# Optimization experiments

Hardware: AMD Instinct MI355X
Metric: run time of the kernel (lower is better)

## Reference

```python
import jax, jax.numpy as jnp
import numpy as np

RH, RW = 40, 64          # render image height/width
SAM_HW = 64              # SAM ViT-H feature map spatial size
FEAT_DIM = 17            # voxel_feature_dim
GAUSSIAN_SEM_WEIGHT = 1.0


def nearest_resize(x, oh, ow):
    # torch F.interpolate mode='nearest': idx = floor(out_idx * in/out)
    ih, iw = x.shape[-2], x.shape[-1]
    ri = jnp.floor(jnp.arange(oh) * (ih / oh)).astype(jnp.int32)
    ci = jnp.floor(jnp.arange(ow) * (iw / ow)).astype(jnp.int32)
    return x[..., ri, :][..., ci]


def bilinear_resize(x, oh, ow):
    # torch bilinear, align_corners=False (half-pixel centers)
    ih, iw = x.shape[-2], x.shape[-1]
    def axis(isz, osz):
        src = (jnp.arange(osz, dtype=x.dtype) + 0.5) * (isz / osz) - 0.5
        i0 = jnp.clip(jnp.floor(src), 0, isz - 1).astype(jnp.int32)
        i1 = jnp.clip(i0 + 1, 0, isz - 1)
        w = jnp.clip(src - i0.astype(x.dtype), 0.0, 1.0)
        return i0, i1, w
    r0, r1, wr = axis(ih, oh)
    c0, c1, wc = axis(iw, ow)
    xr = x[..., r0, :] * (1 - wr)[:, None] + x[..., r1, :] * wr[:, None]
    return xr[..., c0] * (1 - wc) + xr[..., c1] * wc


def quat_to_rot(q):  # q: [N,4] normalized (w,x,y,z)
    w, x, y, z = q[:, 0], q[:, 1], q[:, 2], q[:, 3]
    R = jnp.stack([
        1 - 2 * (y * y + z * z), 2 * (x * y - w * z), 2 * (x * z + w * y),
        2 * (x * y + w * z), 1 - 2 * (x * x + z * z), 2 * (y * z - w * x),
        2 * (x * z - w * y), 2 * (y * z + w * x), 1 - 2 * (x * x + y * y)], -1)
    return R.reshape(-1, 3, 3)


def sam_proj(x, W1, b1, g1, be1, W2, b2, g2, be2, W3, b3):
    # Linear -> LayerNorm -> LeakyReLU (x2) -> Linear, all on last dim
    def ln(h, g, b):
        mu = h.mean(-1, keepdims=True)
        var = ((h - mu) ** 2).mean(-1, keepdims=True)
        return (h - mu) / jnp.sqrt(var + 1e-5) * g + b
    h = jax.nn.leaky_relu(ln(x @ W1.T + b1, g1, be1), 0.01)
    h = jax.nn.leaky_relu(ln(h @ W2.T + b2, g2, be2), 0.01)
    return h @ W3.T + b3


def render_feature_map(xyz, feats, opac, scal, quat, vm, intr):
    # Differentiable EWA Gaussian-splat feature rasterizer (3DGS-style math).
    N = xyz.shape[0]
    Rw, t = vm[:3, :3], vm[:3, 3]
    cam = xyz @ Rw.T + t                      # [N,3] camera coords
    x, y, z = cam[:, 0], cam[:, 1], cam[:, 2]
    fx, fy, cx, cy = intr[0], intr[1], intr[2], intr[3]
    zc = jnp.maximum(z, 1e-3)
    u = fx * x / zc + cx
    v = fy * y / zc + cy
    # 3D covariance Sigma = R S S^T R^T, transformed to camera then projected
    Rq = quat_to_rot(quat)
    M = Rq * scal[:, None, :]
    cov3 = M @ jnp.swapaxes(M, 1, 2)          # [N,3,3]
    covw = jnp.einsum('ij,njk,lk->nil', Rw, cov3, Rw)
    inv_z = 1.0 / zc
    zero = jnp.zeros_like(z)
    J = jnp.stack([
        jnp.stack([fx * inv_z, zero, -fx * x * inv_z ** 2], -1),
        jnp.stack([zero, fy * inv_z, -fy * y * inv_z ** 2], -1)], 1)  # [N,2,3]
    cov2 = jnp.einsum('nij,njk,nlk->nil', J, covw, J)
    a = cov2[:, 0, 0] + 0.3
    bq = cov2[:, 0, 1]
    cc = cov2[:, 1, 1] + 0.3
    det = a * cc - bq * bq
    A, Bc, Cc = cc / det, -bq / det, a / det   # conic (inverse 2D cov)
    xx, yy = jnp.meshgrid(jnp.arange(RW, dtype=xyz.dtype), jnp.arange(RH, dtype=xyz.dtype))
    px, py = xx.reshape(-1), yy.reshape(-1)    # [P]
    dx = u[:, None] - px[None, :]              # [N,P]
    dy = v[:, None] - py[None, :]
    power = -0.5 * (A[:, None] * dx * dx + Cc[:, None] * dy * dy) - Bc[:, None] * dx * dy
    alpha = jnp.minimum(0.99, opac * jnp.exp(jnp.minimum(power, 0.0)))
    alpha = alpha * (z > 0.2).astype(alpha.dtype)[:, None]
    # depth-sorted alpha compositing
    order = jnp.argsort(z)
    a_s = alpha[order]                         # [N,P]
    f_s = feats[order]                         # [N,C]
    T = jnp.concatenate([jnp.ones((1, a_s.shape[1]), a_s.dtype),
                         jnp.cumprod(1.0 - a_s, axis=0)[:-1]], axis=0)
    out = jnp.einsum('np,nc->cp', a_s * T, f_s)  # white_background=False -> bg 0
    return out.reshape(FEAT_DIM, RH, RW)


def _forward(voxel_feats, opacity, sam_embd, sam_features, sam_masks, viewmat,
             intrins, pc_xyz, scales, rots, W1, b1, g1, be1, W2, b2, g2, be2, W3, b3):
    B, C = viewmat.shape[0], viewmat.shape[1]
    scal = jnp.exp(scales)
    quat = rots / jnp.linalg.norm(rots, axis=-1, keepdims=True)
    proj = lambda x: sam_proj(x, W1, b1, g1, be1, W2, b2, g2, be2, W3, b3)
    loss_batch = 0.0
    for b in range(B):
        vf = voxel_feats[b].reshape(-1, FEAT_DIM)
        op = opacity[b].reshape(-1, 1)
        loss_c = 0.0
        for c in range(C):
            fmap = render_feature_map(pc_xyz, vf, op, scal, quat, viewmat[b, c], intrins[b, c])
            # use_sam: L1 between rendered map and projected SAM embedding
            se = nearest_resize(sam_embd[b, c], RH, RW)          # [256,RH,RW]
            sed = proj(se.transpose(1, 2, 0))                    # [RH,RW,17]
            loss_c = loss_c + jnp.abs(fmap.transpose(1, 2, 0) - sed).mean()
            # SAM mask contrastive loss
            sf = sam_features[b, c]                              # [256,64,64]
            ldf = proj(sf.reshape(256, -1).T).T.reshape(FEAT_DIM, SAM_HW, SAM_HW)
            masks = sam_masks[b, c]                              # [M,200,200]
            lsm = nearest_resize(masks, SAM_HW, SAM_HW)          # [M,64,64]
            proto = jnp.einsum('mhw,chw->mc', lsm, ldf)
            proto = proto / jnp.maximum(lsm.sum((1, 2)), 1e-6)[:, None]
            prob = jax.nn.sigmoid(jnp.einsum('mc,chw->mhw', proto, fmap))
            frm = bilinear_resize(masks, RH, RW)
            frm = jnp.where(frm <= 0.5, 0.0, frm)
            bce = frm * jnp.log(prob + 1e-8) + (1 - frm) * jnp.log(1 - prob + 1e-8)
            loss_c = loss_c - bce.mean()
        loss_batch = loss_batch + loss_c / C
    return loss_batch / B * GAUSSIAN_SEM_WEIGHT


def setup_inputs() -> dict:
    key = jax.random.key(0)
    ks = jax.random.split(key, 10)
    vs = 2.0
    gx1 = np.arange(-40.0, 40.0 + vs - 0.1, vs)
    gx = (gx1[:40] + gx1[1:41]) / 2
    gy = gx.copy()
    gz1 = np.arange(-2.4, 13.6 + vs - 0.1, vs)
    gz = (gz1[:8] + gz1[1:9]) / 2
    X, Y, Z = np.meshgrid(gx, gy, gz, indexing='ij')
    pc_xyz = np.stack([X, Y, Z], -1).reshape(-1, 3).astype(np.float32)
    N = pc_xyz.shape[0]  # 12800
    # regular grid: 3-NN mean squared dist = vs^2 -> scales = log(sqrt(vs^2))
    scales = np.full((N, 3), np.log(vs), np.float32)
    rots = np.zeros((N, 4), np.float32); rots[:, 0] = 1.0
    vm = np.zeros((1, 2, 4, 4), np.float32)
    vm[0, :, 0, 0] = vm[0, :, 1, 1] = vm[0, :, 2, 2] = vm[0, :, 3, 3] = 1.0
    vm[0, 0, :3, 3] = [0.0, 0.0, 60.0]
    vm[0, 1, :3, 3] = [2.0, -1.0, 62.0]
    intr = np.tile(np.array([32.0, 20.0, 32.0, 20.0], np.float32), (1, 2, 1))
    inp = {
        'voxel_feats': jax.random.normal(ks[0], (1, N, 17), jnp.float32) * 0.5,
        'opacity': jax.random.uniform(ks[1], (1, N, 1), jnp.float32) * 0.1,
        'sam_embd': jax.random.normal(ks[2], (1, 2, 256, 64, 64), jnp.float32),
        'sam_features': jax.random.normal(ks[3], (1, 2, 256, 64, 64), jnp.float32),
        'sam_masks': (jax.random.uniform(ks[4], (1, 2, 16, 200, 200)) < 0.3).astype(jnp.float32),
        'viewmat': jnp.asarray(vm), 'intrins': jnp.asarray(intr),
        'pc_xyz': jnp.asarray(pc_xyz), 'scales': jnp.asarray(scales), 'rots': jnp.asarray(rots),
        'W1': jax.random.normal(ks[5], (64, 256), jnp.float32) * 0.05,
        'b1': jnp.zeros((64,), jnp.float32),
        'g1': jnp.ones((64,), jnp.float32), 'be1': jnp.zeros((64,), jnp.float32),
        'W2': jax.random.normal(ks[6], (64, 64), jnp.float32) * 0.1,
        'b2': jnp.zeros((64,), jnp.float32),
        'g2': jnp.ones((64,), jnp.float32), 'be2': jnp.zeros((64,), jnp.float32),
        'W3': jax.random.normal(ks[7], (17, 64), jnp.float32) * 0.1,
        'b3': jnp.zeros((17,), jnp.float32),
    }
    return inp


def reference(voxel_feats, opacity, sam_embd, sam_features, sam_masks, viewmat,
              intrins, pc_xyz, scales, rots, W1, b1, g1, be1, W2, b2, g2, be2, W3, b3):
    return _forward(voxel_feats, opacity, sam_embd, sam_features, sam_masks, viewmat,
                    intrins, pc_xyz, scales, rots, W1, b1, g1, be1, W2, b2, g2, be2, W3, b3)
```

## Files before the change

### kernel.cpp

```cpp
#include <hip/hip_runtime.h>
#include <math.h>

#define NPTS   12800
#define P_PIX  2560
#define NC     64
#define CHUNK  200
#define RANK_CHUNK 800
#define MLP_PITCH 264

typedef short short8 __attribute__((ext_vector_type(8)));
typedef float f32x4 __attribute__((ext_vector_type(4)));

__device__ __forceinline__ unsigned short f2bf(float f) {
    unsigned int u = __float_as_uint(f);
    u += 0x7fffu + ((u >> 16) & 1u);
    return (unsigned short)(u >> 16);
}

__global__ __launch_bounds__(256) void init_kernel(int* rnk, float* out, int n) {
    int i = blockIdx.x * 256 + threadIdx.x;
    if (i < n) rnk[i] = 0;
    if (i == 0) out[0] = 0.0f;
}

__global__ __launch_bounds__(256) void prep_kernel(
    const float* __restrict__ xyz, const float* __restrict__ scales,
    const float* __restrict__ rots, const float* __restrict__ opacity,
    const float* __restrict__ viewmat, const float* __restrict__ intrins,
    unsigned long long* __restrict__ keys,
    float* __restrict__ pu, float* __restrict__ pv, float* __restrict__ prad,
    float* __restrict__ phA, float* __restrict__ phC, float* __restrict__ pnB,
    float* __restrict__ pop, int N) {
    int cam = blockIdx.y;
    int i = blockIdx.x * 256 + threadIdx.x;
    if (i >= N) return;
    const float* vm = viewmat + cam * 16;
    const float* it = intrins + cam * 4;
    float fx = it[0], fy = it[1], cx = it[2], cy = it[3];
    float R00 = vm[0], R01 = vm[1], R02 = vm[2], t0 = vm[3];
    float R10 = vm[4], R11 = vm[5], R12 = vm[6], t1 = vm[7];
    float R20 = vm[8], R21 = vm[9], R22 = vm[10], t2 = vm[11];
    float X = xyz[i * 3], Y = xyz[i * 3 + 1], Z = xyz[i * 3 + 2];
    float x = R00 * X + R01 * Y + R02 * Z + t0;
    float y = R10 * X + R11 * Y + R12 * Z + t1;
    float z = R20 * X + R21 * Y + R22 * Z + t2;
    float zc = fmaxf(z, 0.001f);
    float iz = 1.0f / zc;
    float u = fx * x * iz + cx;
    float v = fy * y * iz + cy;
    float qw = rots[i * 4], qx = rots[i * 4 + 1], qy = rots[i * 4 + 2], qz = rots[i * 4 + 3];
    float qn = 1.0f / sqrtf(qw * qw + qx * qx + qy * qy + qz * qz);
    qw *= qn; qx *= qn; qy *= qn; qz *= qn;
    float s0 = expf(scales[i * 3]), s1 = expf(scales[i * 3 + 1]), s2 = expf(scales[i * 3 + 2]);
    float Rq[3][3] = {
        {1 - 2 * (qy * qy + qz * qz), 2 * (qx * qy - qw * qz), 2 * (qx * qz + qw * qy)},
        {2 * (qx * qy + qw * qz), 1 - 2 * (qx * qx + qz * qz), 2 * (qy * qz - qw * qx)},
        {2 * (qx * qz - qw * qy), 2 * (qy * qz + qw * qx), 1 - 2 * (qx * qx + qy * qy)}};
    float M[3][3];
    #pragma unroll
    for (int r = 0; r < 3; ++r) { M[r][0] = Rq[r][0] * s0; M[r][1] = Rq[r][1] * s1; M[r][2] = Rq[r][2] * s2; }
    float c3[3][3];
    #pragma unroll
    for (int a = 0; a < 3; ++a)
        #pragma unroll
        for (int b = 0; b < 3; ++b)
            c3[a][b] = M[a][0] * M[b][0] + M[a][1] * M[b][1] + M[a][2] * M[b][2];
    float Rw[3][3] = {{R00, R01, R02}, {R10, R11, R12}, {R20, R21, R22}};
    float Wt[3][3];
    #pragma unroll
    for (int a = 0; a < 3; ++a)
        #pragma unroll
        for (int b = 0; b < 3; ++b)
            Wt[a][b] = Rw[a][0] * c3[0][b] + Rw[a][1] * c3[1][b] + Rw[a][2] * c3[2][b];
    float cw[3][3];
    #pragma unroll
    for (int a = 0; a < 3; ++a)
        #pragma unroll
        for (int b = 0; b < 3; ++b)
            cw[a][b] = Wt[a][0] * Rw[b][0] + Wt[a][1] * Rw[b][1] + Wt[a][2] * Rw[b][2];
    float j00 = fx * iz, j02 = -fx * x * iz * iz;
    float j11 = fy * iz, j12 = -fy * y * iz * iz;
    float c00 = j00 * j00 * cw[0][0] + 2.0f * j00 * j02 * cw[0][2] + j02 * j02 * cw[2][2];
    float c01 = j00 * j11 * cw[0][1] + j00 * j12 * cw[0][2] + j02 * j11 * cw[2][1] + j02 * j12 * cw[2][2];
    float c11 = j11 * j11 * cw[1][1] + 2.0f * j11 * j12 * cw[1][2] + j12 * j12 * cw[2][2];
    float a = c00 + 0.3f, bq = c01, cc = c11 + 0.3f;
    float det = a * cc - bq * bq;
    float A = cc / det, Bc = -bq / det, Cc = a / det;
    float lmin = 0.5f * ((A + Cc) - sqrtf((A - Cc) * (A - Cc) + 4.0f * Bc * Bc));
    lmin = fmaxf(lmin, 1e-20f);
    float opv = (z > 0.2f) ? opacity[i] : 0.0f;
    float rad = -1.0f;
    if (opv > 0.0f) {
        float tcut = logf(opv) + 18.42f;
        if (tcut > 0.0f) rad = sqrtf(2.0f * tcut / lmin);
    }
    int idx = cam * N + i;
    pu[idx] = u; pv[idx] = v; prad[idx] = rad;
    phA[idx] = -0.5f * A; phC[idx] = -0.5f * Cc; pnB[idx] = -Bc;
    pop[idx] = opv;
    unsigned int zb = __float_as_uint(z);
    zb = (zb & 0x80000000u) ? ~zb : (zb | 0x80000000u);
    keys[idx] = ((unsigned long long)zb << 32) | (unsigned int)i;
}

__global__ __launch_bounds__(256) void rank_kernel(const unsigned long long* __restrict__ keys,
                                                   int* __restrict__ rnk, int N) {
    __shared__ unsigned long long sk[RANK_CHUNK];
    int cam = blockIdx.z;
    const unsigned long long* K = keys + (size_t)cam * N;
    int jbase = blockIdx.y * RANK_CHUNK;
    int jcnt = min(RANK_CHUNK, N - jbase);
    for (int t = threadIdx.x; t < jcnt; t += 256) sk[t] = K[jbase + t];
    __syncthreads();
    int i = blockIdx.x * 256 + threadIdx.x;
    if (i >= N) return;
    unsigned long long ki = K[i];
    int cnt = 0;
    #pragma unroll 8
    for (int j = 0; j < jcnt; ++j) cnt += (sk[j] < ki) ? 1 : 0;
    if (cnt) atomicAdd(rnk + (size_t)cam * N + i, cnt);
}

__global__ __launch_bounds__(256) void scatter_kernel(
    const int* __restrict__ rnk,
    const float* __restrict__ pu, const float* __restrict__ pv, const float* __restrict__ prad,
    const float* __restrict__ phA, const float* __restrict__ phC, const float* __restrict__ pnB,
    const float* __restrict__ pop,
    const float* __restrict__ feats, float* __restrict__ rec, int N) {
    int cam = blockIdx.y;
    int i = blockIdx.x * 256 + threadIdx.x;
    if (i >= N) return;
    int idx = cam * N + i;
    int r = rnk[idx];
    float* d = rec + ((size_t)cam * N + r) * 24;
    d[0] = pu[idx]; d[1] = pv[idx]; d[2] = prad[idx]; d[3] = pop[idx];
    d[4] = phA[idx]; d[5] = phC[idx]; d[6] = pnB[idx];
    const float* f = feats + (size_t)i * 17;
    #pragma unroll
    for (int c = 0; c < 17; ++c) d[7 + c] = f[c];
}

__global__ __launch_bounds__(256) void build_kernel(const float* __restrict__ rec,
                                                    unsigned char* __restrict__ lists,
                                                    int* __restrict__ cnts, int N) {
    int gid = blockIdx.x * 4 + (threadIdx.x >> 6);
    int lane = threadIdx.x & 63;
    int cam = gid / (NC * 40);
    int rem = gid - cam * (NC * 40);
    int ch = rem / 40, row = rem - ch * 40;
    const float* rb = rec + ((size_t)cam * N + ch * CHUNK) * 24;
    unsigned char* L = lists + (size_t)gid * CHUNK;
    float py = (float)row;
    int cnt = 0;
    for (int g = 0; g < CHUNK; g += 64) {
        int n = g + lane;
        bool pass = false;
        if (n < CHUNK) {
            float v = rb[n * 24 + 1], rad = rb[n * 24 + 2];
            pass = fabsf(v - py) <= rad + 0.01f;
        }
        unsigned long long mask = __ballot(pass);
        int pre = __popcll(mask & ((1ull << lane) - 1ull));
        if (pass) L[cnt + pre] = (unsigned char)n;
        cnt += __popcll(mask);
    }
    if (lane == 0) cnts[gid] = cnt;
}

__global__ __launch_bounds__(256) void splat_kernel(const float* __restrict__ rec,
                                                    const unsigned char* __restrict__ lists,
                                                    const int* __restrict__ cnts,
                                                    float* __restrict__ part, int N) {
    __shared__ __align__(16) float4 sRec[CHUNK * 6];
    __shared__ unsigned char sList[4 * CHUNK];
    __shared__ int sCnt[4];
    int cam = blockIdx.z, ch = blockIdx.y, pg = blockIdx.x;
    int tid = threadIdx.x, lane = tid & 63, wv = tid >> 6;
    const float4* src = (const float4*)(rec + ((size_t)cam * N + ch * CHUNK) * 24);
    for (int t = tid; t < CHUNK * 6; t += 256) sRec[t] = src[t];
    int lid0 = (cam * NC + ch) * 40 + pg * 4;
    for (int t = tid; t < 4 * CHUNK; t += 256) {
        int w = t / CHUNK, i = t - w * CHUNK;
        sList[t] = lists[(size_t)(lid0 + w) * CHUNK + i];
    }
    if (tid < 4) sCnt[tid] = cnts[lid0 + tid];
    __syncthreads();
    int row = pg * 4 + wv;
    int cnt = sCnt[wv];
    float px = (float)lane, py = (float)row;
    float T = 1.0f;
    float acc[17];
    #pragma unroll
    for (int c = 0; c < 17; ++c) acc[c] = 0.0f;
    const unsigned char* myL = sList + wv * CHUNK;
    for (int i = 0; i < cnt; ++i) {
        int n = myL[i];
        const float4* rp = sRec + n * 6;
        float4 h  = rp[0];
        float4 b0 = rp[1];
        float dy = h.y - py;
        float dx = h.x - px;
        float hCdy2 = (b0.y * dy) * dy;
        float t1 = fmaf(b0.x, dx, b0.z * dy);
        float power = fminf(fmaf(t1, dx, hCdy2), 0.0f);
        float alpha = fminf(0.99f, h.w * __expf(power));
        float w = alpha * T;
        float4 q1 = rp[2], q2 = rp[3], q3 = rp[4], q4 = rp[5];
        acc[0]  = fmaf(w, b0.w, acc[0]);
        acc[1]  = fmaf(w, q1.x, acc[1]);  acc[2]  = fmaf(w, q1.y, acc[2]);
        acc[3]  = fmaf(w, q1.z, acc[3]);  acc[4]  = fmaf(w, q1.w, acc[4]);
        acc[5]  = fmaf(w, q2.x, acc[5]);  acc[6]  = fmaf(w, q2.y, acc[6]);
        acc[7]  = fmaf(w, q2.z, acc[7]);  acc[8]  = fmaf(w, q2.w, acc[8]);
        acc[9]  = fmaf(w, q3.x, acc[9]);  acc[10] = fmaf(w, q3.y, acc[10]);
        acc[11] = fmaf(w, q3.z, acc[11]); acc[12] = fmaf(w, q3.w, acc[12]);
        acc[13] = fmaf(w, q4.x, acc[13]); acc[14] = fmaf(w, q4.y, acc[14]);
        acc[15] = fmaf(w, q4.z, acc[15]); acc[16] = fmaf(w, q4.w, acc[16]);
        T *= (1.0f - alpha);
    }
    int p0 = row * 64 + lane;
    size_t base = ((size_t)(cam * NC + ch) * 18) * P_PIX;
    part[base + p0] = T;
    #pragma unroll
    for (int c = 0; c < 17; ++c)
        part[base + (size_t)(1 + c) * P_PIX + p0] = acc[c];
}

__global__ __launch_bounds__(256) void tpref_kernel(const float* __restrict__ part,
                                                    float* __restrict__ tpref) {
    int cam = blockIdx.y;
    int p = blockIdx.x * 256 + threadIdx.x;
    float T = 1.0f;
    #pragma unroll 8
    for (int k = 0; k < NC; ++k) {
        tpref[((size_t)(cam * NC + k)) * P_PIX + p] = T;
        T *= part[((size_t)(cam * NC + k) * 18) * P_PIX + p];
    }
}

__global__ __launch_bounds__(256) void combine_kernel(const float* __restrict__ part,
                                                      const float* __restrict__ tpref,
                                                      float* __restrict__ fmap) {
    int idx = blockIdx.x * 256 + threadIdx.x;
    if (idx >= 2 * 17 * P_PIX) return;
    int p = idx % P_PIX;
    int rem = idx / P_PIX;
    int c = rem % 17;
    int cam = rem / 17;
    float acc = 0.0f;
    #pragma unroll 8
    for (int k = 0; k < NC; ++k) {
        float Tp = tpref[((size_t)(cam * NC + k)) * P_PIX + p];
        float S = part[(((size_t)(cam * NC + k)) * 18 + 1 + c) * P_PIX + p];
        acc = fmaf(Tp, S, acc);
    }
    fmap[((size_t)cam * 17 + c) * P_PIX + p] = acc;
}

__global__ __launch_bounds__(256, 2) void mlp_kernel(
    const float* __restrict__ embd, const float* __restrict__ sfeat,
    const float* __restrict__ W1, const float* __restrict__ b1,
    const float* __restrict__ g1, const float* __restrict__ be1,
    const float* __restrict__ W2, const float* __restrict__ b2,
    const float* __restrict__ g2, const float* __restrict__ be2,
    const float* __restrict__ W3, const float* __restrict__ b3,
    float* __restrict__ sed, float* __restrict__ ldf) {
    __shared__ __align__(16) unsigned short smem[2 * 64 * MLP_PITCH];
    unsigned short* sX = smem;
    unsigned short* sW = smem + 64 * MLP_PITCH;
    int tid = threadIdx.x, lane = tid & 63, wv = tid >> 6;
    int m = lane & 15, kq = lane >> 4, q4 = kq * 4;
    int tile = blockIdx.x;
    const float* xbase;
    if (tile < 80) {
        int cam = tile / 40; int r = tile - cam * 40;
        int ri = (r * 8) / 5;
        xbase = embd + (size_t)cam * 256 * 4096 + ri * 64;
    } else {
        int tt = tile - 80; int cam = tt >> 6;
        xbase = sfeat + (size_t)cam * 256 * 4096 + (tt & 63) * 64;
    }
    const float4* xf4 = (const float4*)xbase;
    for (int idx = tid; idx < 4096; idx += 256) {
        int k = idx >> 4, q = idx & 15;
        float4 xv = xf4[(size_t)k * 1024 + q];
        int r = q * 4;
        sX[(r + 0) * MLP_PITCH + k] = f2bf(xv.x);
        sX[(r + 1) * MLP_PITCH + k] = f2bf(xv.y);
        sX[(r + 2) * MLP_PITCH + k] = f2bf(xv.z);
        sX[(r + 3) * MLP_PITCH + k] = f2bf(xv.w);
    }
    const float4* wf4 = (const float4*)W1;
    for (int idx = tid; idx < 4096; idx += 256) {
        float4 wvv = wf4[idx];
        int n = idx >> 6, kk = (idx & 63) * 4;
        uint2 pk;
        pk.x = (unsigned int)f2bf(wvv.x) | ((unsigned int)f2bf(wvv.y) << 16);
        pk.y = (unsigned int)f2bf(wvv.z) | ((unsigned int)f2bf(wvv.w) << 16);
        *(uint2*)&sW[n * MLP_PITCH + kk] = pk;
    }
    float b1v[4], g1v[4], be1v[4], b2v[4], g2v[4], be2v[4];
    #pragma unroll
    for (int nt = 0; nt < 4; ++nt) {
        int c = nt * 16 + m;
        b1v[nt] = b1[c]; g1v[nt] = g1[c]; be1v[nt] = be1[c];
        b2v[nt] = b2[c]; g2v[nt] = g2[c]; be2v[nt] = be2[c];
    }
    __syncthreads();
    f32x4 acc[4];
    #pragma unroll
    for (int nt = 0; nt < 4; ++nt) acc[nt] = (f32x4){0.f, 0.f, 0.f, 0.f};
    const unsigned short* aptr = sX + (wv * 16 + m) * MLP_PITCH + kq * 8;
    const unsigned short* bptr = sW + m * MLP_PITCH + kq * 8;
    #pragma unroll
    for (int ks = 0; ks < 8; ++ks) {
        short8 af = *(const short8*)(aptr + ks * 32);
        #pragma unroll
        for (int nt = 0; nt < 4; ++nt) {
            short8 bf = *(const short8*)(bptr + nt * 16 * MLP_PITCH + ks * 32);
            acc[nt] = __builtin_amdgcn_mfma_f32_16x16x32_bf16(af, bf, acc[nt], 0, 0, 0);
        }
    }
    __syncthreads();
    unsigned short* hbuf  = smem + wv * 16 * 72;
    unsigned short* hbuf2 = smem + (4 + wv) * 16 * 72;
    unsigned short* W2b = sW;
    unsigned short* W3b = sW + 64 * 72;
    for (int i = tid; i < 4096; i += 256)
        W2b[(i >> 6) * 72 + (i & 63)] = f2bf(W2[i]);
    for (int i = tid; i < 2048; i += 256) {
        int n = i >> 6, k = i & 63;
        W3b[n * 72 + k] = (n < 17) ? f2bf(W3[n * 64 + k]) : 0;
    }
    #pragma unroll
    for (int rg = 0; rg < 4; ++rg) {
        float h0 = acc[0][rg] + b1v[0], h1 = acc[1][rg] + b1v[1];
        float h2 = acc[2][rg] + b1v[2], h3 = acc[3][rg] + b1v[3];
        float s = (h0 + h1) + (h2 + h3);
        s += __shfl_xor(s, 1); s += __shfl_xor(s, 2);
        s += __shfl_xor(s, 4); s += __shfl_xor(s, 8);
        float mu = s * (1.0f / 64.0f);
        float d0 = h0 - mu, d1 = h1 - mu, d2 = h2 - mu, d3 = h3 - mu;
        float vs = (d0 * d0 + d1 * d1) + (d2 * d2 + d3 * d3);
        vs += __shfl_xor(vs, 1); vs += __shfl_xor(vs, 2);
        vs += __shfl_xor(vs, 4); vs += __shfl_xor(vs, 8);
        float rstd = 1.0f / sqrtf(vs * (1.0f / 64.0f) + 1e-5f);
        float hn0 = d0 * rstd * g1v[0] + be1v[0]; hn0 = fmaxf(hn0, 0.01f * hn0);
        float hn1 = d1 * rstd * g1v[1] + be1v[1]; hn1 = fmaxf(hn1, 0.01f * hn1);
        float hn2 = d2 * rstd * g1v[2] + be1v[2]; hn2 = fmaxf(hn2, 0.01f * hn2);
        float hn3 = d3 * rstd * g1v[3] + be1v[3]; hn3 = fmaxf(hn3, 0.01f * hn3);
        int rr = (q4 + rg) * 72 + m;
        hbuf[rr] = f2bf(hn0); hbuf[rr + 16] = f2bf(hn1);
        hbuf[rr + 32] = f2bf(hn2); hbuf[rr + 48] = f2bf(hn3);
    }
    __syncthreads();
    f32x4 acc2[4];
    #pragma unroll
    for (int nt = 0; nt < 4; ++nt) acc2[nt] = (f32x4){0.f, 0.f, 0.f, 0.f};
    const unsigned short* a2p = hbuf + m * 72 + kq * 8;
    #pragma unroll
    for (int ks = 0; ks < 2; ++ks) {
        short8 af = *(const short8*)(a2p + ks * 32);
        #pragma unroll
        for (int nt = 0; nt < 4; ++nt) {
            short8 bf = *(const short8*)(W2b + (nt * 16 + m) * 72 + kq * 8 + ks * 32);
            acc2[nt] = __builtin_amdgcn_mfma_f32_16x16x32_bf16(af, bf, acc2[nt], 0, 0, 0);
        }
    }
    #pragma unroll
    for (int rg = 0; rg < 4; ++rg) {
        float h0 = acc2[0][rg] + b2v[0], h1 = acc2[1][rg] + b2v[1];
        float h2 = acc2[2][rg] + b2v[2], h3 = acc2[3][rg] + b2v[3];
        float s = (h0 + h1) + (h2 + h3);
        s += __shfl_xor(s, 1); s += __shfl_xor(s, 2);
        s += __shfl_xor(s, 4); s += __shfl_xor(s, 8);
        float mu = s * (1.0f / 64.0f);
        float d0 = h0 - mu, d1 = h1 - mu, d2 = h2 - mu, d3 = h3 - mu;
        float vs = (d0 * d0 + d1 * d1) + (d2 * d2 + d3 * d3);
        vs += __shfl_xor(vs, 1); vs += __shfl_xor(vs, 2);
        vs += __shfl_xor(vs, 4); vs += __shfl_xor(vs, 8);
        float rstd = 1.0f / sqrtf(vs * (1.0f / 64.0f) + 1e-5f);
        float hn0 = d0 * rstd * g2v[0] + be2v[0]; hn0 = fmaxf(hn0, 0.01f * hn0);
        float hn1 = d1 * rstd * g2v[1] + be2v[1]; hn1 = fmaxf(hn1, 0.01f * hn1);
        float hn2 = d2 * rstd * g2v[2] + be2v[2]; hn2 = fmaxf(hn2, 0.01f * hn2);
        float hn3 = d3 * rstd * g2v[3] + be2v[3]; hn3 = fmaxf(hn3, 0.01f * hn3);
        int rr = (q4 + rg) * 72 + m;
        hbuf2[rr] = f2bf(hn0); hbuf2[rr + 16] = f2bf(hn1);
        hbuf2[rr + 32] = f2bf(hn2); hbuf2[rr + 48] = f2bf(hn3);
    }
    f32x4 acc3[2];
    acc3[0] = (f32x4){0.f, 0.f, 0.f, 0.f};
    acc3[1] = (f32x4){0.f, 0.f, 0.f, 0.f};
    const unsigned short* a3p = hbuf2 + m * 72 + kq * 8;
    #pragma unroll
    for (int ks = 0; ks < 2; ++ks) {
        short8 af = *(const short8*)(a3p + ks * 32);
        #pragma unroll
        for (int nt = 0; nt < 2; ++nt) {
            short8 bf = *(const short8*)(W3b + (nt * 16 + m) * 72 + kq * 8 + ks * 32);
            acc3[nt] = __builtin_amdgcn_mfma_f32_16x16x32_bf16(af, bf, acc3[nt], 0, 0, 0);
        }
    }
    #pragma unroll
    for (int nt = 0; nt < 2; ++nt) {
        int c = nt * 16 + m;
        if (c < 17) {
            float b3v = b3[c];
            #pragma unroll
            for (int rg = 0; rg < 4; ++rg) {
                int row = tile * 64 + wv * 16 + q4 + rg;
                float val = acc3[nt][rg] + b3v;
                if (row < 5120) {
                    int cam = row / 2560; int p = row - cam * 2560;
                    sed[((size_t)cam * 2560 + p) * 17 + c] = val;
                } else {
                    int rr = row - 5120; int cam = rr >> 12; int t = rr & 4095;
                    ldf[((size_t)cam * 17 + c) * 4096 + t] = val;
                }
            }
        }
    }
}

__global__ __launch_bounds__(256) void proto_kernel(const float* __restrict__ masks,
                                                    const float* __restrict__ ldf,
                                                    float* __restrict__ proto) {
    int cam = blockIdx.y, m = blockIdx.x;
    const float* M = masks + ((size_t)cam * 16 + m) * 40000;
    float acc[18];
    #pragma unroll
    for (int j = 0; j < 18; ++j) acc[j] = 0.0f;
    for (int t = threadIdx.x; t < 4096; t += 256) {
        int h = t >> 6, w = t & 63;
        int rh = (h * 25) >> 3, rw = (w * 25) >> 3;
        float lv = M[rh * 200 + rw];
        if (lv != 0.0f) {
            acc[17] += lv;
            const float* L = ldf + (size_t)cam * 17 * 4096 + t;
            #pragma unroll
            for (int c = 0; c < 17; ++c) acc[c] = fmaf(lv, L[(size_t)c * 4096], acc[c]);
        }
    }
    __shared__ float red[4][18];
    int lane = threadIdx.x & 63, wv = threadIdx.x >> 6;
    #pragma unroll
    for (int j = 0; j < 18; ++j) {
        float v = acc[j];
        #pragma unroll
        for (int o = 32; o; o >>= 1) v += __shfl_xor(v, o);
        if (lane == 0) red[wv][j] = v;
    }
    __syncthreads();
    if (threadIdx.x < 17) {
        float sacc = red[0][threadIdx.x] + red[1][threadIdx.x] + red[2][threadIdx.x] + red[3][threadIdx.x];
        float ms = red[0][17] + red[1][17] + red[2][17] + red[3][17];
        proto[((size_t)cam * 16 + m) * 17 + threadIdx.x] = sacc / fmaxf(ms, 1e-6f);
    }
}

__device__ __forceinline__ void block_atomic_add(float v, float* target) {
    #pragma unroll
    for (int o = 32; o; o >>= 1) v += __shfl_xor(v, o);
    __shared__ float sred[4];
    int lane = threadIdx.x & 63, wv = threadIdx.x >> 6;
    if (lane == 0) sred[wv] = v;
    __syncthreads();
    if (threadIdx.x == 0) atomicAdd(target, sred[0] + sred[1] + sred[2] + sred[3]);
}

__global__ __launch_bounds__(256) void bce_kernel(const float* __restrict__ masks,
                                                  const float* __restrict__ proto,
                                                  const float* __restrict__ fmap,
                                                  float* __restrict__ out) {
    int idx = blockIdx.x * 256 + threadIdx.x;
    int p = idx % P_PIX;
    int rem = idx / P_PIX;
    int m = rem & 15, cam = rem >> 4;
    const float* pr = proto + ((size_t)cam * 16 + m) * 17;
    float sdot = 0;
    #pragma unroll
    for (int c = 0; c < 17; ++c)
        sdot = fmaf(pr[c], fmap[((size_t)cam * 17 + c) * P_PIX + p], sdot);
    float prob = 1.0f / (1.0f + expf(-sdot));
    int px = p & 63, py = p >> 6;
    float src_r = (py + 0.5f) * 5.0f - 0.5f;
    float src_c = (px + 0.5f) * 3.125f - 0.5f;
    int r0 = (int)fminf(fmaxf(floorf(src_r), 0.0f), 199.0f);
    int r1 = min(r0 + 1, 199);
    float wr = fminf(fmaxf(src_r - (float)r0, 0.0f), 1.0f);
    int c0 = (int)fminf(fmaxf(floorf(src_c), 0.0f), 199.0f);
    int c1 = min(c0 + 1, 199);
    float wc = fminf(fmaxf(src_c - (float)c0, 0.0f), 1.0f);
    const float* M = masks + ((size_t)cam * 16 + m) * 40000;
    float v00 = M[r0 * 200 + c0], v01 = M[r0 * 200 + c1];
    float v10 = M[r1 * 200 + c0], v11 = M[r1 * 200 + c1];
    float xr0 = v00 * (1.0f - wr) + v10 * wr;
    float xr1 = v01 * (1.0f - wr) + v11 * wr;
    float frm = xr0 * (1.0f - wc) + xr1 * wc;
    frm = (frm <= 0.5f) ? 0.0f : frm;
    float bce = frm * logf(prob + 1e-8f) + (1.0f - frm) * logf(1.0f - prob + 1e-8f);
    block_atomic_add(bce * (-1.0f / (16.0f * 2560.0f * 2.0f)), out);
}

__global__ __launch_bounds__(256) void l1_kernel(const float* __restrict__ fmap,
                                                 const float* __restrict__ sed,
                                                 float* __restrict__ out) {
    int idx = blockIdx.x * 256 + threadIdx.x;
    float ssum = 0;
    if (idx < 2 * P_PIX) {
        int p = idx % P_PIX, cam = idx / P_PIX;
        #pragma unroll
        for (int c = 0; c < 17; ++c) {
            float dv = fmap[((size_t)cam * 17 + c) * P_PIX + p] - sed[((size_t)cam * P_PIX + p) * 17 + c];
            ssum += fabsf(dv);
        }
    }
    block_atomic_add(ssum * (1.0f / (43520.0f * 2.0f)), out);
}

extern "C" void kernel_launch(void* const* d_in, const int* in_sizes, int n_in,
                              void* d_out, int out_size, void* d_ws, size_t ws_size,
                              hipStream_t stream) {
    const float* voxel_feats = (const float*)d_in[0];
    const float* opacity     = (const float*)d_in[1];
    const float* sam_embd    = (const float*)d_in[2];
    const float* sam_features= (const float*)d_in[3];
    const float* sam_masks   = (const float*)d_in[4];
    const float* viewmat     = (const float*)d_in[5];
    const float* intrins     = (const float*)d_in[6];
    const float* pc_xyz      = (const float*)d_in[7];
    const float* scales      = (const float*)d_in[8];
    const float* rots        = (const float*)d_in[9];
    const float* W1 = (const float*)d_in[10], *b1 = (const float*)d_in[11];
    const float* g1 = (const float*)d_in[12], *be1 = (const float*)d_in[13];
    const float* W2 = (const float*)d_in[14], *b2 = (const float*)d_in[15];
    const float* g2 = (const float*)d_in[16], *be2 = (const float*)d_in[17];
    const float* W3 = (const float*)d_in[18], *b3 = (const float*)d_in[19];
    float* out = (float*)d_out;
    const int N = in_sizes[7] / 3;

    char* w = (char*)d_ws;
    size_t off = 0;
    auto alloc = [&](size_t bytes) -> void* {
        off = (off + 255) & ~(size_t)255;
        void* p = w + off; off += bytes; return p;
    };
    int* rnk  = (int*)alloc((size_t)2 * N * sizeof(int));
    unsigned long long* keys = (unsigned long long*)alloc((size_t)2 * N * 8);
    float* params = (float*)alloc((size_t)7 * 2 * N * 4);
    float* pu  = params,           *pv  = params + 2 * N,  *prad = params + 4 * N;
    float* phA = params + 6 * N,   *phC = params + 8 * N,  *pnB  = params + 10 * N;
    float* pop = params + 12 * N;
    float* rec   = (float*)alloc((size_t)2 * N * 24 * 4);
    float* part  = (float*)alloc((size_t)2 * NC * 18 * P_PIX * 4);
    float* tpref = (float*)alloc((size_t)2 * NC * P_PIX * 4);
    float* fmap  = (float*)alloc((size_t)2 * 17 * P_PIX * 4);
    float* sed   = (float*)alloc((size_t)2 * P_PIX * 17 * 4);
    float* ldf   = (float*)alloc((size_t)2 * 17 * 4096 * 4);
    float* proto = (float*)alloc((size_t)2 * 16 * 17 * 4);
    unsigned char* lists = (unsigned char*)alloc((size_t)2 * NC * 40 * CHUNK);
    int* cnts = (int*)alloc((size_t)2 * NC * 40 * sizeof(int));

    init_kernel<<<(2 * N + 255) / 256, 256, 0, stream>>>(rnk, out, 2 * N);
    dim3 gprep((N + 255) / 256, 2);
    prep_kernel<<<gprep, 256, 0, stream>>>(pc_xyz, scales, rots, opacity, viewmat, intrins,
                                           keys, pu, pv, prad, phA, phC, pnB, pop, N);
    dim3 grank((N + 255) / 256, (N + RANK_CHUNK - 1) / RANK_CHUNK, 2);
    rank_kernel<<<grank, 256, 0, stream>>>(keys, rnk, N);
    scatter_kernel<<<gprep, 256, 0, stream>>>(rnk, pu, pv, prad, phA, phC, pnB, pop,
                                              voxel_feats, rec, N);
    build_kernel<<<2 * NC * 40 / 4, 256, 0, stream>>>(rec, lists, cnts, N);
    dim3 gsplat(10, NC, 2);
    splat_kernel<<<gsplat, 256, 0, stream>>>(rec, lists, cnts, part, N);
    dim3 gtp(P_PIX / 256, 2);
    tpref_kernel<<<gtp, 256, 0, stream>>>(part, tpref);
    combine_kernel<<<(2 * 17 * P_PIX + 255) / 256, 256, 0, stream>>>(part, tpref, fmap);
    mlp_kernel<<<208, 256, 0, stream>>>(sam_embd, sam_features, W1, b1, g1, be1,
                                        W2, b2, g2, be2, W3, b3, sed, ldf);
    dim3 gproto(16, 2);
    proto_kernel<<<gproto, 256, 0, stream>>>(sam_masks, ldf, proto);
    bce_kernel<<<(2 * 16 * P_PIX) / 256, 256, 0, stream>>>(sam_masks, proto, fmap, out);
    l1_kernel<<<(2 * P_PIX + 255) / 256, 256, 0, stream>>>(fmap, sed, out);
}
```

Before: 236.3 us.

## Fuse init/tpref/l1 kernels, enlarge chunks, register-tile rank, compact splat record

Folds the rank-buffer zeroing into prep, the transmittance prefix into combine, and the L1 loss into the BCE kernel, removing three launches and the tpref buffer. Halves the depth-chunk count by doubling chunk size, which moves list indices to 16-bit, and adds a separate compact (v, radius) array so the list-build pass reads 8 bytes per point instead of strided records. The rank kernel now compares each shared key against four per-thread keys to raise reuse, and the splat inner loop uses packed two-wide FMAs over a tighter record layout. BCE switches to fast exp/log intrinsics, which slightly changes numerics, and larger chunks mean longer serial per-wave loops with fewer blocks.

```diff
diff --git a/kernel.cpp b/kernel.cpp
--- a/kernel.cpp
+++ b/kernel.cpp
@@ -3,24 +3,20 @@
 
 #define NPTS   12800
 #define P_PIX  2560
-#define NC     64
-#define CHUNK  200
+#define NC     32
+#define CHUNK  400
 #define RANK_CHUNK 800
+#define RT     4
 #define MLP_PITCH 264
 
 typedef short short8 __attribute__((ext_vector_type(8)));
 typedef float f32x4 __attribute__((ext_vector_type(4)));
+typedef float f32x2 __attribute__((ext_vector_type(2)));
 
 __device__ __forceinline__ unsigned short f2bf(float f) {
     unsigned int u = __float_as_uint(f);
     u += 0x7fffu + ((u >> 16) & 1u);
     return (unsigned short)(u >> 16);
-}
-
-__global__ __launch_bounds__(256) void init_kernel(int* rnk, float* out, int n) {
-    int i = blockIdx.x * 256 + threadIdx.x;
-    if (i < n) rnk[i] = 0;
-    if (i == 0) out[0] = 0.0f;
 }
 
 __global__ __launch_bounds__(256) void prep_kernel(
@@ -30,10 +26,13 @@
     unsigned long long* __restrict__ keys,
     float* __restrict__ pu, float* __restrict__ pv, float* __restrict__ prad,
     float* __restrict__ phA, float* __restrict__ phC, float* __restrict__ pnB,
-    float* __restrict__ pop, int N) {
+    float* __restrict__ pop, int* __restrict__ rnk, float* __restrict__ out, int N) {
     int cam = blockIdx.y;
     int i = blockIdx.x * 256 + threadIdx.x;
     if (i >= N) return;
+    int idx = cam * N + i;
+    rnk[idx] = 0;
+    if (idx == 0) out[0] = 0.0f;
     const float* vm = viewmat + cam * 16;
     const float* it = intrins + cam * 4;
     float fx = it[0], fy = it[1], cx = it[2], cy = it[3];
@@ -94,7 +93,6 @@
         float tcut = logf(opv) + 18.42f;
         if (tcut > 0.0f) rad = sqrtf(2.0f * tcut / lmin);
     }
-    int idx = cam * N + i;
     pu[idx] = u; pv[idx] = v; prad[idx] = rad;
     phA[idx] = -0.5f * A; phC[idx] = -0.5f * Cc; pnB[idx] = -Bc;
     pop[idx] = opv;
@@ -112,13 +110,26 @@
     int jcnt = min(RANK_CHUNK, N - jbase);
     for (int t = threadIdx.x; t < jcnt; t += 256) sk[t] = K[jbase + t];
     __syncthreads();
-    int i = blockIdx.x * 256 + threadIdx.x;
-    if (i >= N) return;
-    unsigned long long ki = K[i];
-    int cnt = 0;
-    #pragma unroll 8
-    for (int j = 0; j < jcnt; ++j) cnt += (sk[j] < ki) ? 1 : 0;
-    if (cnt) atomicAdd(rnk + (size_t)cam * N + i, cnt);
+    int i0 = blockIdx.x * (256 * RT) + threadIdx.x;
+    unsigned long long ki[RT];
+    int cnt[RT];
+    #pragma unroll
+    for (int t = 0; t < RT; ++t) {
+        int i = i0 + t * 256;
+        ki[t] = (i < N) ? K[i] : 0xFFFFFFFFFFFFFFFFull;
+        cnt[t] = 0;
+    }
+    #pragma unroll 4
+    for (int j = 0; j < jcnt; ++j) {
+        unsigned long long kj = sk[j];
+        #pragma unroll
+        for (int t = 0; t < RT; ++t) cnt[t] += (kj < ki[t]) ? 1 : 0;
+    }
+    #pragma unroll
+    for (int t = 0; t < RT; ++t) {
+        int i = i0 + t * 256;
+        if (i < N && cnt[t]) atomicAdd(rnk + (size_t)cam * N + i, cnt[t]);
+    }
 }
 
 __global__ __launch_bounds__(256) void scatter_kernel(
@@ -126,119 +137,110 @@
     const float* __restrict__ pu, const float* __restrict__ pv, const float* __restrict__ prad,
     const float* __restrict__ phA, const float* __restrict__ phC, const float* __restrict__ pnB,
     const float* __restrict__ pop,
-    const float* __restrict__ feats, float* __restrict__ rec, int N) {
+    const float* __restrict__ feats, float* __restrict__ rec, float2* __restrict__ vr, int N) {
     int cam = blockIdx.y;
     int i = blockIdx.x * 256 + threadIdx.x;
     if (i >= N) return;
     int idx = cam * N + i;
     int r = rnk[idx];
     float* d = rec + ((size_t)cam * N + r) * 24;
-    d[0] = pu[idx]; d[1] = pv[idx]; d[2] = prad[idx]; d[3] = pop[idx];
-    d[4] = phA[idx]; d[5] = phC[idx]; d[6] = pnB[idx];
+    d[0] = pu[idx]; d[1] = pv[idx]; d[2] = pop[idx]; d[3] = phA[idx];
+    d[4] = phC[idx]; d[5] = pnB[idx];
     const float* f = feats + (size_t)i * 17;
     #pragma unroll
-    for (int c = 0; c < 17; ++c) d[7 + c] = f[c];
-}
-
-__global__ __launch_bounds__(256) void build_kernel(const float* __restrict__ rec,
-                                                    unsigned char* __restrict__ lists,
+    for (int c = 0; c < 17; ++c) d[6 + c] = f[c];
+    d[23] = 0.0f;
+    vr[(size_t)cam * N + r] = make_float2(pv[idx], prad[idx]);
+}
+
+__global__ __launch_bounds__(256) void build_kernel(const float2* __restrict__ vr,
+                                                    unsigned short* __restrict__ lists,
                                                     int* __restrict__ cnts, int N) {
     int gid = blockIdx.x * 4 + (threadIdx.x >> 6);
     int lane = threadIdx.x & 63;
     int cam = gid / (NC * 40);
     int rem = gid - cam * (NC * 40);
     int ch = rem / 40, row = rem - ch * 40;
-    const float* rb = rec + ((size_t)cam * N + ch * CHUNK) * 24;
-    unsigned char* L = lists + (size_t)gid * CHUNK;
+    const float2* V = vr + (size_t)cam * N + ch * CHUNK;
+    unsigned short* L = lists + (size_t)gid * CHUNK;
     float py = (float)row;
     int cnt = 0;
     for (int g = 0; g < CHUNK; g += 64) {
         int n = g + lane;
         bool pass = false;
         if (n < CHUNK) {
-            float v = rb[n * 24 + 1], rad = rb[n * 24 + 2];
-            pass = fabsf(v - py) <= rad + 0.01f;
+            float2 t = V[n];
+            pass = fabsf(t.x - py) <= t.y + 0.01f;
         }
         unsigned long long mask = __ballot(pass);
         int pre = __popcll(mask & ((1ull << lane) - 1ull));
-        if (pass) L[cnt + pre] = (unsigned char)n;
+        if (pass) L[cnt + pre] = (unsigned short)n;
         cnt += __popcll(mask);
     }
     if (lane == 0) cnts[gid] = cnt;
 }
 
 __global__ __launch_bounds__(256) void splat_kernel(const float* __restrict__ rec,
-                                                    const unsigned char* __restrict__ lists,
+                                                    const unsigned short* __restrict__ lists,
                                                     const int* __restrict__ cnts,
                                                     float* __restrict__ part, int N) {
     __shared__ __align__(16) float4 sRec[CHUNK * 6];
-    __shared__ unsigned char sList[4 * CHUNK];
+    __shared__ unsigned short sList[4 * CHUNK];
     __shared__ int sCnt[4];
     int cam = blockIdx.z, ch = blockIdx.y, pg = blockIdx.x;
     int tid = threadIdx.x, lane = tid & 63, wv = tid >> 6;
     const float4* src = (const float4*)(rec + ((size_t)cam * N + ch * CHUNK) * 24);
     for (int t = tid; t < CHUNK * 6; t += 256) sRec[t] = src[t];
     int lid0 = (cam * NC + ch) * 40 + pg * 4;
-    for (int t = tid; t < 4 * CHUNK; t += 256) {
-        int w = t / CHUNK, i = t - w * CHUNK;
-        sList[t] = lists[(size_t)(lid0 + w) * CHUNK + i];
-    }
+    const unsigned int* Lb = (const unsigned int*)(lists + (size_t)lid0 * CHUNK);
+    unsigned int* sL = (unsigned int*)sList;
+    for (int t = tid; t < 2 * CHUNK; t += 256) sL[t] = Lb[t];
     if (tid < 4) sCnt[tid] = cnts[lid0 + tid];
     __syncthreads();
     int row = pg * 4 + wv;
     int cnt = sCnt[wv];
     float px = (float)lane, py = (float)row;
     float T = 1.0f;
-    float acc[17];
-    #pragma unroll
-    for (int c = 0; c < 17; ++c) acc[c] = 0.0f;
-    const unsigned char* myL = sList + wv * CHUNK;
+    f32x2 acc[9];
+    #pragma unroll
+    for (int j = 0; j < 9; ++j) acc[j] = (f32x2){0.f, 0.f};
+    const unsigned short* myL = sList + wv * CHUNK;
     for (int i = 0; i < cnt; ++i) {
         int n = myL[i];
         const float4* rp = sRec + n * 6;
-        float4 h  = rp[0];
-        float4 b0 = rp[1];
-        float dy = h.y - py;
-        float dx = h.x - px;
-        float hCdy2 = (b0.y * dy) * dy;
-        float t1 = fmaf(b0.x, dx, b0.z * dy);
-        float power = fminf(fmaf(t1, dx, hCdy2), 0.0f);
-        float alpha = fminf(0.99f, h.w * __expf(power));
+        float4 q0 = rp[0];
+        float4 q1 = rp[1];
+        float dx = q0.x - px, dy = q0.y - py;
+        float t1 = (q1.y * dx) * dy;
+        t1 = fmaf(q1.x * dy, dy, t1);
+        float power = fminf(fmaf(q0.w * dx, dx, t1), 0.0f);
+        float alpha = fminf(0.99f, q0.z * __expf(power));
         float w = alpha * T;
-        float4 q1 = rp[2], q2 = rp[3], q3 = rp[4], q4 = rp[5];
-        acc[0]  = fmaf(w, b0.w, acc[0]);
-        acc[1]  = fmaf(w, q1.x, acc[1]);  acc[2]  = fmaf(w, q1.y, acc[2]);
-        acc[3]  = fmaf(w, q1.z, acc[3]);  acc[4]  = fmaf(w, q1.w, acc[4]);
-        acc[5]  = fmaf(w, q2.x, acc[5]);  acc[6]  = fmaf(w, q2.y, acc[6]);
-        acc[7]  = fmaf(w, q2.z, acc[7]);  acc[8]  = fmaf(w, q2.w, acc[8]);
-        acc[9]  = fmaf(w, q3.x, acc[9]);  acc[10] = fmaf(w, q3.y, acc[10]);
-        acc[11] = fmaf(w, q3.z, acc[11]); acc[12] = fmaf(w, q3.w, acc[12]);
-        acc[13] = fmaf(w, q4.x, acc[13]); acc[14] = fmaf(w, q4.y, acc[14]);
-        acc[15] = fmaf(w, q4.z, acc[15]); acc[16] = fmaf(w, q4.w, acc[16]);
+        f32x2 w2 = (f32x2){w, w};
+        float4 q2 = rp[2], q3 = rp[3], q4 = rp[4], q5 = rp[5];
+        acc[0] += w2 * (f32x2){q1.z, q1.w};
+        acc[1] += w2 * (f32x2){q2.x, q2.y};
+        acc[2] += w2 * (f32x2){q2.z, q2.w};
+        acc[3] += w2 * (f32x2){q3.x, q3.y};
+        acc[4] += w2 * (f32x2){q3.z, q3.w};
+        acc[5] += w2 * (f32x2){q4.x, q4.y};
+        acc[6] += w2 * (f32x2){q4.z, q4.w};
+        acc[7] += w2 * (f32x2){q5.x, q5.y};
+        acc[8] += w2 * (f32x2){q5.z, q5.w};
         T *= (1.0f - alpha);
     }
     int p0 = row * 64 + lane;
     size_t base = ((size_t)(cam * NC + ch) * 18) * P_PIX;
     part[base + p0] = T;
     #pragma unroll
-    for (int c = 0; c < 17; ++c)
-        part[base + (size_t)(1 + c) * P_PIX + p0] = acc[c];
-}
-
-__global__ __launch_bounds__(256) void tpref_kernel(const float* __restrict__ part,
-                                                    float* __restrict__ tpref) {
-    int cam = blockIdx.y;
-    int p = blockIdx.x * 256 + threadIdx.x;
-    float T = 1.0f;
-    #pragma unroll 8
-    for (int k = 0; k < NC; ++k) {
-        tpref[((size_t)(cam * NC + k)) * P_PIX + p] = T;
-        T *= part[((size_t)(cam * NC + k) * 18) * P_PIX + p];
-    }
+    for (int j = 0; j < 8; ++j) {
+        part[base + (size_t)(1 + 2 * j) * P_PIX + p0] = acc[j][0];
+        part[base + (size_t)(2 + 2 * j) * P_PIX + p0] = acc[j][1];
+    }
+    part[base + (size_t)17 * P_PIX + p0] = acc[8][0];
 }
 
 __global__ __launch_bounds__(256) void combine_kernel(const float* __restrict__ part,
-                                                      const float* __restrict__ tpref,
                                                       float* __restrict__ fmap) {
     int idx = blockIdx.x * 256 + threadIdx.x;
     if (idx >= 2 * 17 * P_PIX) return;
@@ -246,12 +248,14 @@
     int rem = idx / P_PIX;
     int c = rem % 17;
     int cam = rem / 17;
-    float acc = 0.0f;
+    float acc = 0.0f, Tp = 1.0f;
     #pragma unroll 8
     for (int k = 0; k < NC; ++k) {
-        float Tp = tpref[((size_t)(cam * NC + k)) * P_PIX + p];
-        float S = part[(((size_t)(cam * NC + k)) * 18 + 1 + c) * P_PIX + p];
+        size_t base = ((size_t)(cam * NC + k) * 18) * P_PIX + p;
+        float Tk = part[base];
+        float S  = part[base + (size_t)(1 + c) * P_PIX];
         acc = fmaf(Tp, S, acc);
+        Tp *= Tk;
     }
     fmap[((size_t)cam * 17 + c) * P_PIX + p] = acc;
 }
@@ -470,17 +474,20 @@
 __global__ __launch_bounds__(256) void bce_kernel(const float* __restrict__ masks,
                                                   const float* __restrict__ proto,
                                                   const float* __restrict__ fmap,
+                                                  const float* __restrict__ sed,
                                                   float* __restrict__ out) {
     int idx = blockIdx.x * 256 + threadIdx.x;
     int p = idx % P_PIX;
     int rem = idx / P_PIX;
     int m = rem & 15, cam = rem >> 4;
     const float* pr = proto + ((size_t)cam * 16 + m) * 17;
+    float f[17];
+    #pragma unroll
+    for (int c = 0; c < 17; ++c) f[c] = fmap[((size_t)cam * 17 + c) * P_PIX + p];
     float sdot = 0;
     #pragma unroll
-    for (int c = 0; c < 17; ++c)
-        sdot = fmaf(pr[c], fmap[((size_t)cam * 17 + c) * P_PIX + p], sdot);
-    float prob = 1.0f / (1.0f + expf(-sdot));
+    for (int c = 0; c < 17; ++c) sdot = fmaf(pr[c], f[c], sdot);
+    float prob = 1.0f / (1.0f + __expf(-sdot));
     int px = p & 63, py = p >> 6;
     float src_r = (py + 0.5f) * 5.0f - 0.5f;
     float src_c = (px + 0.5f) * 3.125f - 0.5f;
@@ -497,24 +504,16 @@
     float xr1 = v01 * (1.0f - wr) + v11 * wr;
     float frm = xr0 * (1.0f - wc) + xr1 * wc;
     frm = (frm <= 0.5f) ? 0.0f : frm;
-    float bce = frm * logf(prob + 1e-8f) + (1.0f - frm) * logf(1.0f - prob + 1e-8f);
-    block_atomic_add(bce * (-1.0f / (16.0f * 2560.0f * 2.0f)), out);
-}
-
-__global__ __launch_bounds__(256) void l1_kernel(const float* __restrict__ fmap,
-                                                 const float* __restrict__ sed,
-                                                 float* __restrict__ out) {
-    int idx = blockIdx.x * 256 + threadIdx.x;
-    float ssum = 0;
-    if (idx < 2 * P_PIX) {
-        int p = idx % P_PIX, cam = idx / P_PIX;
-        #pragma unroll
-        for (int c = 0; c < 17; ++c) {
-            float dv = fmap[((size_t)cam * 17 + c) * P_PIX + p] - sed[((size_t)cam * P_PIX + p) * 17 + c];
-            ssum += fabsf(dv);
-        }
-    }
-    block_atomic_add(ssum * (1.0f / (43520.0f * 2.0f)), out);
+    float bce = frm * __logf(prob + 1e-8f) + (1.0f - frm) * __logf(1.0f - prob + 1e-8f);
+    float val = bce * (-1.0f / (16.0f * 2560.0f * 2.0f));
+    if (m == 0) {
+        float ssum = 0.0f;
+        const float* sp = sed + ((size_t)cam * P_PIX + p) * 17;
+        #pragma unroll
+        for (int c = 0; c < 17; ++c) ssum += fabsf(f[c] - sp[c]);
+        val += ssum * (1.0f / (43520.0f * 2.0f));
+    }
+    block_atomic_add(val, out);
 }
 
 extern "C" void kernel_launch(void* const* d_in, const int* in_sizes, int n_in,
@@ -551,33 +550,29 @@
     float* phA = params + 6 * N,   *phC = params + 8 * N,  *pnB  = params + 10 * N;
     float* pop = params + 12 * N;
     float* rec   = (float*)alloc((size_t)2 * N * 24 * 4);
+    float2* vr   = (float2*)alloc((size_t)2 * N * 8);
     float* part  = (float*)alloc((size_t)2 * NC * 18 * P_PIX * 4);
-    float* tpref = (float*)alloc((size_t)2 * NC * P_PIX * 4);
     float* fmap  = (float*)alloc((size_t)2 * 17 * P_PIX * 4);
     float* sed   = (float*)alloc((size_t)2 * P_PIX * 17 * 4);
     float* ldf   = (float*)alloc((size_t)2 * 17 * 4096 * 4);
     float* proto = (float*)alloc((size_t)2 * 16 * 17 * 4);
-    unsigned char* lists = (unsigned char*)alloc((size_t)2 * NC * 40 * CHUNK);
+    unsigned short* lists = (unsigned short*)alloc((size_t)2 * NC * 40 * CHUNK * 2);
     int* cnts = (int*)alloc((size_t)2 * NC * 40 * sizeof(int));
 
-    init_kernel<<<(2 * N + 255) / 256, 256, 0, stream>>>(rnk, out, 2 * N);
     dim3 gprep((N + 255) / 256, 2);
     prep_kernel<<<gprep, 256, 0, stream>>>(pc_xyz, scales, rots, opacity, viewmat, intrins,
-                                           keys, pu, pv, prad, phA, phC, pnB, pop, N);
-    dim3 grank((N + 255) / 256, (N + RANK_CHUNK - 1) / RANK_CHUNK, 2);
+                                           keys, pu, pv, prad, phA, phC, pnB, pop, rnk, out, N);
+    dim3 grank((N + 256 * RT - 1) / (256 * RT), (N + RANK_CHUNK - 1) / RANK_CHUNK, 2);
     rank_kernel<<<grank, 256, 0, stream>>>(keys, rnk, N);
     scatter_kernel<<<gprep, 256, 0, stream>>>(rnk, pu, pv, prad, phA, phC, pnB, pop,
-                                              voxel_feats, rec, N);
-    build_kernel<<<2 * NC * 40 / 4, 256, 0, stream>>>(rec, lists, cnts, N);
+                                              voxel_feats, rec, vr, N);
+    build_kernel<<<2 * NC * 40 / 4, 256, 0, stream>>>(vr, lists, cnts, N);
     dim3 gsplat(10, NC, 2);
     splat_kernel<<<gsplat, 256, 0, stream>>>(rec, lists, cnts, part, N);
-    dim3 gtp(P_PIX / 256, 2);
-    tpref_kernel<<<gtp, 256, 0, stream>>>(part, tpref);
-    combine_kernel<<<(2 * 17 * P_PIX + 255) / 256, 256, 0, stream>>>(part, tpref, fmap);
     mlp_kernel<<<208, 256, 0, stream>>>(sam_embd, sam_features, W1, b1, g1, be1,
                                         W2, b2, g2, be2, W3, b3, sed, ldf);
+    combine_kernel<<<(2 * 17 * P_PIX + 255) / 256, 256, 0, stream>>>(part, fmap);
     dim3 gproto(16, 2);
     proto_kernel<<<gproto, 256, 0, stream>>>(sam_masks, ldf, proto);
-    bce_kernel<<<(2 * 16 * P_PIX) / 256, 256, 0, stream>>>(sam_masks, proto, fmap, out);
-    l1_kernel<<<(2 * P_PIX + 255) / 256, 256, 0, stream>>>(fmap, sed, out);
-}
+    bce_kernel<<<(2 * 16 * P_PIX) / 256, 256, 0, stream>>>(sam_masks, proto, fmap, sed, out);
+}
```

After: 233.5 us. Within noise of the previous version (-1.2%).
